# Kernel optimization log

Measured on AMD Instinct MI355X. Metric: run time of the kernel, lower is better.

The kernel has to match this reference:

```python
import jax, jax.numpy as jnp
import numpy as np

B_SZ, SEQ, ENC = 8, 768, 21
PRED = 192
N_HIPPO = 256
MULTISCALE = [1, 2, 4]
MODES = 32  # min(32, min(pred_len, seq_len)//2)


def _transition(N):
    Q = np.arange(N, dtype=np.float64)
    R = (2 * Q + 1)[:, None]
    j, i = np.meshgrid(Q, Q)
    A = np.where(i < j, -1.0, (-1.0) ** (i - j + 1)) * R
    Bv = (-1.0) ** Q[:, None] * R
    return A, Bv


def _hippo_discrete(N, dt):
    # scipy cont2discrete bilinear (Tustin, alpha=0.5)
    A, Bv = _transition(N)
    I = np.eye(N)
    M = I - (dt / 2.0) * A
    Ad = np.linalg.solve(M, I + (dt / 2.0) * A)
    Bd = np.linalg.solve(M, dt * Bv).squeeze(-1)
    return (jnp.asarray(Ad, jnp.float32), jnp.asarray(Bd, jnp.float32))


def _eval_matrix(N, dt):
    # ss.eval_legendre(arange(N)[:,None], 1-2*vals).T  -> (len(vals), N)
    vals = np.arange(0.0, 1.0, dt)
    x = 1.0 - 2.0 * vals
    P = np.zeros((len(vals), N), dtype=np.float64)
    P[:, 0] = 1.0
    if N > 1:
        P[:, 1] = x
    for n in range(1, N - 1):
        P[:, n + 1] = ((2 * n + 1) * x * P[:, n] - n * P[:, n - 1]) / (n + 1)
    return jnp.asarray(P, jnp.float32)


def _legt(x, A, Bv):
    # x: (B, E, L) -> HiPPO coeffs (B, E, N, L) via linear recurrence
    fs = jnp.moveaxis(x, -1, 0)  # (L, B, E)
    c0 = jnp.zeros(x.shape[:-1] + (A.shape[0],), x.dtype)

    def step(c, f):
        c = c @ A.T + f[..., None] * Bv
        return c, c

    _, cs = jax.lax.scan(step, c0, fs)  # (L, B, E, N)
    return jnp.moveaxis(cs, 0, -1)  # (B, E, N, L)


def _spectral(x, wr, wi):
    # x: (B, E, N_in, L); wr/wi: (N_in, N_out, MODES)
    L = x.shape[-1]
    xft = jnp.fft.rfft(x)
    a = xft[..., :MODES]
    o_re = jnp.einsum('bjix,iox->bjox', a.real, wr) - jnp.einsum('bjix,iox->bjox', a.imag, wi)
    o_im = jnp.einsum('bjix,iox->bjox', a.real, wi) + jnp.einsum('bjix,iox->bjox', a.imag, wr)
    o = jax.lax.complex(o_re, o_im)
    pad = jnp.zeros(o.shape[:-1] + (L // 2 + 1 - MODES,), o.dtype)
    return jnp.fft.irfft(jnp.concatenate([o, pad], axis=-1), n=L)


def _forward(x_enc, affine_weight, affine_bias, spec_wr, spec_wi, mlp_w, mlp_b):
    means = jax.lax.stop_gradient(jnp.mean(x_enc, axis=1, keepdims=True))
    xc = x_enc - means
    stdev = jax.lax.stop_gradient(jnp.sqrt(jnp.var(xc, axis=1, keepdims=True) + 1e-5))
    xc = xc / stdev
    xc = xc * affine_weight + affine_bias

    x_decs = []
    for i, m in enumerate(MULTISCALE):
        dt = 1.0 / PRED / m
        A, Bv = _hippo_discrete(N_HIPPO, dt)
        ev = _eval_matrix(N_HIPPO, dt)  # (m*PRED, N)
        x_in = xc[:, -m * PRED:]  # (B, L, E)
        c = _legt(jnp.transpose(x_in, (0, 2, 1)), A, Bv)  # (B, E, N, L)
        out1 = _spectral(c, spec_wr[i], spec_wi[i])  # (B, E, N, L)
        # seq_len >= pred_len branch: take time index PRED-1 along L
        x_dec_c = out1[:, :, :, PRED - 1].swapaxes(-1, -1)  # (B, E, N) after transpose(2,3) + index
        x_dec_c = out1.swapaxes(2, 3)[:, :, PRED - 1, :]  # (B, E, N)
        x_dec = x_dec_c @ ev[-PRED:, :].T  # (B, E, PRED)
        x_decs.append(x_dec)

    xd = jnp.stack(x_decs, axis=-1)  # (B, E, PRED, 3)
    xd = jnp.einsum('beps,os->bepo', xd, mlp_w) + mlp_b  # Linear(3,1)
    xd = jnp.transpose(xd[..., 0], (0, 2, 1))  # (B, PRED, E)
    xd = (xd - affine_bias) / (affine_weight + 1e-10)
    xd = xd * stdev + means
    return xd


def setup_inputs() -> dict:
    key = jax.random.key(0)
    ks = jax.random.split(key, 8)
    scale = 1.0 / (N_HIPPO * N_HIPPO)
    return {
        'x_enc': jax.random.normal(ks[0], (B_SZ, SEQ, ENC), jnp.float32),
        'x_mark_enc': jax.random.normal(ks[1], (B_SZ, SEQ, 4), jnp.float32),
        'x_dec_true': jax.random.normal(ks[2], (B_SZ, 240, ENC), jnp.float32),
        'x_mark_dec': jax.random.normal(ks[3], (B_SZ, 240, 4), jnp.float32),
        'affine_weight': jnp.ones((1, 1, ENC), jnp.float32),
        'affine_bias': jnp.zeros((1, 1, ENC), jnp.float32),
        'spec_wr': scale * jax.random.uniform(ks[4], (3, N_HIPPO, N_HIPPO, MODES), jnp.float32),
        'spec_wi': scale * jax.random.uniform(ks[5], (3, N_HIPPO, N_HIPPO, MODES), jnp.float32),
        'mlp_w': jax.random.normal(ks[6], (1, 3), jnp.float32) * 0.3,
        'mlp_b': jnp.zeros((1,), jnp.float32),
    }


def reference(x_enc, x_mark_enc, x_dec_true, x_mark_dec, affine_weight, affine_bias,
              spec_wr, spec_wi, mlp_w, mlp_b):
    # x_mark_enc / x_dec_true / x_mark_dec are unused by the forecast path (as in torch).
    return _forward(x_enc, affine_weight, affine_bias, spec_wr, spec_wi, mlp_w, mlp_b)
```

## Files before the change

### kernel.cpp

```cpp
#include <hip/hip_runtime.h>
#include <vector>
#include <cmath>
#include <cstring>

#define PI_D 3.14159265358979323846

typedef unsigned short ushort_t;
typedef __attribute__((ext_vector_type(8))) short bf16x8;
typedef __attribute__((ext_vector_type(4))) float f32x4;

#define CF_TRIG_F 0
#define CF_EVP_F  192
#define CF_FLOATS 147648
#define CU_USHORTS 688128
#define CONST_BYTES (CF_FLOATS*4 + CU_USHORTS*2)

#define OFF_XCT   0
#define OFF_MEANS 129024
#define OFF_STD   129280
#define OFF_OUT1  129536
#define OFF_XP1P  258560
#define OFF_PART  1161728
#define OFF_AHI   5290496
#define OFF_ALO   9419264
#define OFF_FB2   13548032
#define OFF_YF    26130944
#define OFF_CFALL 40581632

static const int L_S[3] = {192, 384, 768};


static inline unsigned short h_f2b(float v) {
  unsigned int u; memcpy(&u, &v, 4);
  unsigned int r = (u + 0x7FFF + ((u >> 16) & 1)) >> 16;
  return (unsigned short)r;
}
static inline float h_b2f(unsigned short h) {
  unsigned int u = (unsigned int)h << 16; float f; memcpy(&f, &u, 4); return f;
}

static unsigned char g_consts[CONST_BYTES];

static void compute_consts_host(unsigned char* blob) {
  float* outf = (float*)blob;
  ushort_t* outu = (ushort_t*)(blob + CF_FLOATS * 4);
  const int N = 256;
  for (int s = 0; s < 3; ++s) {
    const int L = L_S[s];
    const int m = 1 << s;
    const double dt = 1.0 / 192.0 / (double)m;

    for (int k = 0; k < 32; ++k) {
      double th = 2.0 * PI_D * (double)k * 191.0 / (double)L;
      outf[CF_TRIG_F + s * 64 + 2 * k]     = (float)cos(th);
      outf[CF_TRIG_F + s * 64 + 2 * k + 1] = (float)sin(th);
    }
    for (int r = 0; r < 192; ++r) {
      int irow = L - 192 + r;
      double x = 1.0 - 2.0 * ((double)irow * dt);
      float* dst = outf + CF_EVP_F + ((size_t)s * 192 + r) * 256;
      double pm1 = 1.0, pc = x;
      dst[0] = 1.0f; dst[1] = (float)x;
      for (int n = 1; n < N - 1; ++n) {
        double pn = ((2.0 * n + 1.0) * x * pc - (double)n * pm1) / (double)(n + 1);
        pm1 = pc; pc = pn;
        dst[n + 1] = (float)pn;
      }
    }
    const int W = N + 257;
    std::vector<double> G((size_t)N * W);
    for (int i = 0; i < N; ++i) {
      double R = 2.0 * i + 1.0;
      for (int j = 0; j < N; ++j) {
        double a = (i < j) ? -R : ((((i - j + 1) & 1) ? -R : R));
        G[(size_t)i * W + j]     = (i == j ? 1.0 : 0.0) - 0.5 * dt * a;
        G[(size_t)i * W + N + j] = (i == j ? 1.0 : 0.0) + 0.5 * dt * a;
      }
      G[(size_t)i * W + N + 256] = dt * (((i & 1) ? -R : R));
    }
    for (int k = 0; k < N; ++k) {
      int piv = k; double best = fabs(G[(size_t)k * W + k]);
      for (int r = k + 1; r < N; ++r) {
        double v = fabs(G[(size_t)r * W + k]);
        if (v > best) { best = v; piv = r; }
      }
      if (piv != k)
        for (int c = k; c < W; ++c) std::swap(G[(size_t)k * W + c], G[(size_t)piv * W + c]);
      double inv = 1.0 / G[(size_t)k * W + k];
      for (int r = k + 1; r < N; ++r) {
        double f = G[(size_t)r * W + k] * inv;
        if (f != 0.0) {
          double* Rr = &G[(size_t)r * W];
          const double* Rk = &G[(size_t)k * W];
          for (int c = k; c < W; ++c) Rr[c] -= f * Rk[c];
        }
      }
    }
    std::vector<double> X((size_t)N * 257);
    for (int k = N - 1; k >= 0; --k) {
      double inv = 1.0 / G[(size_t)k * W + k];
      const double* Rk = &G[(size_t)k * W];
      for (int c = 0; c < 257; ++c) {
        double v = Rk[N + c];
        for (int j = k + 1; j < N; ++j) v -= Rk[j] * X[(size_t)j * 257 + c];
        X[(size_t)k * 257 + c] = v * inv;
      }
    }
    std::vector<double> Ad((size_t)N * N), kvec(N), knew(N);
    for (int i = 0; i < N; ++i)
      for (int j = 0; j < N; ++j)
        Ad[(size_t)i * N + j] = (double)(float)X[(size_t)i * 257 + j];
    for (int i = 0; i < N; ++i) kvec[i] = (double)(float)X[(size_t)i * 257 + 256];

    ushort_t* fkt = outu + 98304 * ((1 << s) - 1);
    for (int d = 0; d < L; ++d) {
      if (d > 0) {
        for (int i = 0; i < N; ++i) {
          const double* row = &Ad[(size_t)i * N];
          double acc = 0.0;
          for (int j = 0; j < N; ++j) acc += row[j] * kvec[j];
          knew[i] = acc;
        }
        kvec.swap(knew);
      }
      for (int n = 0; n < N; ++n) {
        float kv = (float)kvec[n];
        unsigned short hi = h_f2b(kv);
        unsigned short lo = h_f2b(kv - h_b2f(hi));
        size_t base = ((size_t)((d >> 5) * 16 + (n >> 4)) * 2) * 512
                    + (size_t)((d & 31) >> 3) * 128 + (size_t)(n & 15) * 8 + (d & 7);
        fkt[base]       = hi;
        fkt[base + 512] = lo;
      }
    }
  }
}

static bool  g_dev_ok  = false;
static void* g_dev_ptr = nullptr;

namespace {
struct ConstInit {
  ConstInit() {
    compute_consts_host(g_consts);
    void* p = nullptr;
    if (hipMalloc(&p, CONST_BYTES) == hipSuccess && p != nullptr) {
      if (hipMemcpy(p, g_consts, CONST_BYTES, hipMemcpyHostToDevice) == hipSuccess) {
        g_dev_ptr = p;
        g_dev_ok  = true;
      } else {
        (void)hipFree(p);
      }
    }
    (void)hipHostRegister((void*)g_consts, sizeof(g_consts), hipHostRegisterDefault);
  }
};
static ConstInit g_const_init;
}

__device__ inline unsigned short f2b(float v) {
  unsigned int u = __float_as_uint(v);
  unsigned int r = (u + 0x7FFF + ((u >> 16) & 1)) >> 16;
  return (unsigned short)r;
}
__device__ inline float b2f(unsigned short h) {
  return __uint_as_float((unsigned int)h << 16);
}
__device__ inline unsigned int pack2(float a, float b) {
  return (unsigned int)f2b(a) | ((unsigned int)f2b(b) << 16);
}

__device__ inline float blockReduceSum(float v) {
  __shared__ float sm[4];
  #pragma unroll
  for (int off = 32; off > 0; off >>= 1) v += __shfl_down(v, off);
  int wid = threadIdx.x >> 6, lane = threadIdx.x & 63;
  if (lane == 0) sm[wid] = v;
  __syncthreads();
  if (threadIdx.x == 0) sm[0] = sm[0] + sm[1] + sm[2] + sm[3];
  __syncthreads();
  float r = sm[0];
  __syncthreads();
  return r;
}

__global__ __launch_bounds__(256) void norm_kernel(
    const float* __restrict__ x_enc, const float* __restrict__ aw,
    const float* __restrict__ ab, float* __restrict__ xcT,
    float* __restrict__ means, float* __restrict__ stdev) {
  int bj = blockIdx.x; int b = bj / 21, j = bj % 21;
  const float* xp = x_enc + (size_t)b * 768 * 21 + j;
  int tid = threadIdx.x;
  float lv[3]; float s = 0.f;
  #pragma unroll
  for (int i = 0; i < 3; ++i) { lv[i] = xp[(size_t)(tid + 256 * i) * 21]; s += lv[i]; }
  float tot = blockReduceSum(s);
  float mean = tot * (1.0f / 768.0f);
  float v = 0.f;
  #pragma unroll
  for (int i = 0; i < 3; ++i) { float d = lv[i] - mean; v += d * d; }
  float totv = blockReduceSum(v);
  float sd = sqrtf(totv * (1.0f / 768.0f) + 1e-5f);
  if (tid == 0) { means[bj] = mean; stdev[bj] = sd; }
  float wj = aw[j], bjv = ab[j];
  #pragma unroll
  for (int i = 0; i < 3; ++i)
    xcT[(size_t)bj * 768 + tid + 256 * i] = ((lv[i] - mean) / sd) * wj + bjv;
}

__global__ __launch_bounds__(256) void xp1_kernel(
    const float* __restrict__ xcT, double2* __restrict__ P) {
  int tid = blockIdx.x * 256 + threadIdx.x;
  if (tid >= 5376 * 42) return;
  int nk = tid % 5376, cg = tid / 5376;
  int scale = (cg < 6) ? 0 : (cg < 18 ? 1 : 2);
  int c = cg - 6 * ((1 << scale) - 1);
  int L = 192 << scale;
  int bj = nk >> 5, k = nk & 31;
  const float* x = xcT + (size_t)bj * 768 + (768 - L);
  int u0 = c * 32;
  double ang = -2.0 * PI_D * (double)((k * u0) % L) / (double)L;
  float re = (float)cos(ang), im = (float)sin(ang);
  double wang = -2.0 * PI_D * (double)k / (double)L;
  float cw = (float)cos(wang), sw = (float)sin(wang);
  double sre = 0.0, sim = 0.0;
  #pragma unroll 8
  for (int j = 0; j < 32; ++j) {
    float xv = x[u0 + j];
    sre += (double)(xv * re); sim += (double)(xv * im);
    float nr = re * cw - im * sw, ni = re * sw + im * cw;
    re = nr; im = ni;
  }
  P[(size_t)cg * 5376 + nk] = make_double2(sre, sim);
}

__global__ __launch_bounds__(256) void xp2_kernel(
    const float* __restrict__ xcT, const double2* __restrict__ P,
    ushort_t* __restrict__ YF) {
  int tid = blockIdx.x * 256 + threadIdx.x;
  if (tid >= 5376 * 42) return;
  int nk = tid % 5376, cg = tid / 5376;
  int scale = (cg < 6) ? 0 : (cg < 18 ? 1 : 2);
  int cbase = 6 * ((1 << scale) - 1);
  int c = cg - cbase;
  int L = 192 << scale;
  ushort_t* FA = YF + (size_t)4128768 * ((1 << scale) - 1);
  int bj = nk >> 5, k = nk & 31;
  const float* x = xcT + (size_t)bj * 768 + (768 - L);
  double bre = 0.0, bim = 0.0;
  for (int cc = cbase; cc < cg; ++cc) {
    double2 p = P[(size_t)cc * 5376 + nk];
    bre += p.x; bim += p.y;
  }
  int u0 = c * 32;
  double ang = -2.0 * PI_D * (double)((k * u0) % L) / (double)L;
  float ure = (float)cos(ang), uim = (float)sin(ang);
  double wang = -2.0 * PI_D * (double)k / (double)L;
  float cw = (float)cos(wang), sw = (float)sin(wang);
  int d0 = L - 1 - u0;
  double angd = -2.0 * PI_D * (double)((k * d0) % L) / (double)L;
  float dre = (float)cos(angd), dim = (float)sin(angd);

  float vre_buf[32], vim_buf[32];
  #pragma unroll
  for (int j = 0; j < 32; ++j) {
    float xv = x[u0 + j];
    bre += (double)(xv * ure); bim += (double)(xv * uim);
    float brf = (float)bre, bif = (float)bim;
    int m = 31 - j;
    vre_buf[m] = dre * brf - dim * bif;
    vim_buf[m] = dre * bif + dim * brf;
    float t1 = ure * cw - uim * sw, t2 = ure * sw + uim * cw;
    ure = t1; uim = t2;
    float t3 = dre * cw + dim * sw, t4 = dim * cw - dre * sw;
    dre = t3; dim = t4;
  }

  int nK0 = L >> 5;
  int K0 = (d0 - 31) >> 5;
  int rre = bj * 64 + k * 2;
  int rim = rre + 1;
  size_t baseRe = (((size_t)(rre >> 4) * nK0 + K0) * 2) * 512 + (size_t)(rre & 15) * 8;
  size_t baseIm = (((size_t)(rim >> 4) * nK0 + K0) * 2) * 512 + (size_t)(rim & 15) * 8;
  #pragma unroll
  for (int q = 0; q < 4; ++q) {
    float f0 = vre_buf[q*8+0], f1 = vre_buf[q*8+1], f2 = vre_buf[q*8+2], f3 = vre_buf[q*8+3];
    float f4 = vre_buf[q*8+4], f5 = vre_buf[q*8+5], f6 = vre_buf[q*8+6], f7 = vre_buf[q*8+7];
    uint4 vh = make_uint4(pack2(f0,f1), pack2(f2,f3), pack2(f4,f5), pack2(f6,f7));
    uint4 vl = make_uint4(pack2(f0-b2f(f2b(f0)), f1-b2f(f2b(f1))),
                          pack2(f2-b2f(f2b(f2)), f3-b2f(f2b(f3))),
                          pack2(f4-b2f(f2b(f4)), f5-b2f(f2b(f5))),
                          pack2(f6-b2f(f2b(f6)), f7-b2f(f2b(f7))));
    *(uint4*)(FA + baseRe + q*128)       = vh;
    *(uint4*)(FA + baseRe + 512 + q*128) = vl;
  }
  #pragma unroll
  for (int q = 0; q < 4; ++q) {
    float f0 = vim_buf[q*8+0], f1 = vim_buf[q*8+1], f2 = vim_buf[q*8+2], f3 = vim_buf[q*8+3];
    float f4 = vim_buf[q*8+4], f5 = vim_buf[q*8+5], f6 = vim_buf[q*8+6], f7 = vim_buf[q*8+7];
    uint4 vh = make_uint4(pack2(f0,f1), pack2(f2,f3), pack2(f4,f5), pack2(f6,f7));
    uint4 vl = make_uint4(pack2(f0-b2f(f2b(f0)), f1-b2f(f2b(f1))),
                          pack2(f2-b2f(f2b(f2)), f3-b2f(f2b(f3))),
                          pack2(f4-b2f(f2b(f4)), f5-b2f(f2b(f5))),
                          pack2(f6-b2f(f2b(f6)), f7-b2f(f2b(f7))));
    *(uint4*)(FA + baseIm + q*128)       = vh;
    *(uint4*)(FA + baseIm + 512 + q*128) = vl;
  }
}

__global__ __launch_bounds__(768, 3) void gemm1_wb(
    const ushort_t* __restrict__ YF, const ushort_t* __restrict__ KTall,
    ushort_t* __restrict__ AHI, ushort_t* __restrict__ ALO,
    const float* __restrict__ wrS_all, const float* __restrict__ wiS_all,
    const float* __restrict__ trig_all, ushort_t* __restrict__ FB2_all) {
  if (blockIdx.x < 384) {
    if (threadIdx.x >= 512) return;
    int wbid = blockIdx.x;
    int of  = wbid & 15;
    int nsb = (wbid >> 4) & 7;
    int s   = wbid >> 7;
    const float* wrS = wrS_all + (size_t)s * 256 * 256 * 32;
    const float* wiS = wiS_all + (size_t)s * 256 * 256 * 32;
    const float* trig = trig_all + s * 64;
    ushort_t* FB2 = FB2_all + (size_t)s * 8388608;
    int L = 192 << s;
    int t = threadIdx.x;
    int lgk = t >> 7;
    int e   = t & 7;
    int om  = (t >> 3) & 15;
    int nstate = nsb * 32 + lgk * 8 + e;
    int o = of * 16 + om;
    const float* wrp = wrS + ((size_t)nstate * 256 + o) * 32;
    const float* wip = wiS + ((size_t)nstate * 256 + o) * 32;
    float invL = 1.0f / (float)L;
    #pragma unroll 4
    for (int k = 0; k < 32; ++k) {
      float ck = trig[2 * k], sk = trig[2 * k + 1];
      float fk = (k == 0 ? 1.0f : 2.0f) * invL;
      float wr = wrp[k], wi = wip[k];
      float vre = fk * (wr * ck - wi * sk);
      float vim = fk * (-wi * ck - wr * sk);
      int qre = (k * 2) * 8 + nsb;
      size_t bre = ((size_t)(qre * 16 + of) * 2) * 512 + t;
      size_t bim = ((size_t)((qre + 8) * 16 + of) * 2) * 512 + t;
      unsigned short hre = f2b(vre), him = f2b(vim);
      FB2[bre]       = hre;
      FB2[bre + 512] = f2b(vre - b2f(hre));
      FB2[bim]       = him;
      FB2[bim + 512] = f2b(vim - b2f(him));
    }
    return;
  }

  const int gb = blockIdx.x - 384;
  const int s = gb / 112;
  const int bx = gb % 112;
  const int K = 192 << s;
  const ushort_t* FA = YF + (size_t)4128768 * ((1 << s) - 1);
  const ushort_t* FB = KTall + (size_t)98304 * ((1 << s) - 1);
  ushort_t* Chi = AHI + (size_t)2752512 * s;
  ushort_t* Clo = ALO + (size_t)2752512 * s;

  const int wave = threadIdx.x >> 6;
  const int lane = threadIdx.x & 63;
  const int li = lane & 15, lg = lane >> 4;
  const int mh = wave >> 2;
  const int nw = wave & 3;
  const int bn = nw * 64;
  const int nK0 = K >> 5;
  const int strip = bx * 6 + mh * 2;
  const int nf0 = nw * 4;

  bf16x8 aH0[2], aL0[2], bH0[4], bL0[4];
  bf16x8 aH1[2], aL1[2], bH1[4], bL1[4];
  f32x4 acc[2][4] = {};

  #define G1_LOAD(AH, AL, BH, BL, K0_) {                                      \
    _Pragma("unroll")                                                         \
    for (int st = 0; st < 2; ++st) {                                          \
      size_t fa = ((size_t)((strip + st) * nK0 + (K0_)) * 2) * 512 + lane * 8;\
      AH[st] = *(const bf16x8*)(FA + fa);                                     \
      AL[st] = *(const bf16x8*)(FA + fa + 512);                               \
    }                                                                         \
    _Pragma("unroll")                                                         \
    for (int nf = 0; nf < 4; ++nf) {                                          \
      size_t fb = ((size_t)((K0_) * 16 + nf0 + nf) * 2) * 512 + lane * 8;     \
      BH[nf] = *(const bf16x8*)(FB + fb);                                     \
      BL[nf] = *(const bf16x8*)(FB + fb + 512);                               \
    } }

  #define G1_MFMA(AH, AL, BH, BL) {                                          \
    _Pragma("unroll")                                                        \
    for (int st = 0; st < 2; ++st)                                           \
      _Pragma("unroll")                                                      \
      for (int nf = 0; nf < 4; ++nf) {                                       \
        acc[st][nf] = __builtin_amdgcn_mfma_f32_16x16x32_bf16(AH[st], BH[nf], acc[st][nf], 0, 0, 0); \
        acc[st][nf] = __builtin_amdgcn_mfma_f32_16x16x32_bf16(AH[st], BL[nf], acc[st][nf], 0, 0, 0); \
        acc[st][nf] = __builtin_amdgcn_mfma_f32_16x16x32_bf16(AL[st], BH[nf], acc[st][nf], 0, 0, 0); \
      } }

  G1_LOAD(aH0, aL0, bH0, bL0, 0);
  for (int K0 = 0; K0 < nK0; K0 += 2) {
    G1_LOAD(aH1, aL1, bH1, bL1, K0 + 1);
    G1_MFMA(aH0, aL0, bH0, bL0);
    if (K0 + 2 < nK0) G1_LOAD(aH0, aL0, bH0, bL0, K0 + 2);
    G1_MFMA(aH1, aL1, bH1, bL1);
  }
  #undef G1_LOAD
  #undef G1_MFMA

  #pragma unroll
  for (int st = 0; st < 2; ++st) {
    #pragma unroll
    for (int r = 0; r < 4; ++r) {
      int row = (strip + st) * 16 + lg * 4 + r;
      #pragma unroll
      for (int nf = 0; nf < 4; ++nf) {
        int col = bn + nf * 16 + li;
        float v = acc[st][nf][r];
        unsigned short hi = f2b(v);
        Chi[(size_t)row * 256 + col] = hi;
        Clo[(size_t)row * 256 + col] = f2b(v - b2f(hi));
      }
    }
  }
}

__global__ __launch_bounds__(256) void gemm2_mfma(
    const ushort_t* __restrict__ AHI, const ushort_t* __restrict__ ALO,
    const ushort_t* __restrict__ FB2_all, float* __restrict__ PART) {
  const int zz = blockIdx.z;
  const int s = zz >> 5;
  const int z = zz & 31;
  const ushort_t* Ahi = AHI + (size_t)2752512 * s;
  const ushort_t* Alo = ALO + (size_t)2752512 * s;
  const ushort_t* FB2 = FB2_all + (size_t)s * 8388608;
  float* C = PART + (size_t)s * 1376256 + (size_t)z * 43008;

  const int wave = threadIdx.x >> 6;
  const int lane = threadIdx.x & 63;
  const int li = lane & 15, lg = lane >> 4;
  const int bm = blockIdx.y * 64;
  const int bn = blockIdx.x * 64;
  const int nf0 = blockIdx.x * 4;
  const int ks = z * 512;

  const int rowA = bm + wave * 16 + li;
  const bool aok = (rowA < 168);
  const size_t aoff = (size_t)(aok ? rowA : 0) * 16384;

  bf16x8 aH0, aL0, bH0[4], bL0[4];
  bf16x8 aH1, aL1, bH1[4], bL1[4];
  f32x4 acc[4] = {};

  #define G2_LOAD(AH, AL, BH, BL, KC_) {                                   \
    int kc_ = (KC_) + lg * 8;                                              \
    if (aok) { AH = *(const bf16x8*)(Ahi + aoff + kc_);                    \
               AL = *(const bf16x8*)(Alo + aoff + kc_); }                  \
    else     { AH = (bf16x8)(short)0; AL = (bf16x8)(short)0; }             \
    int q_ = (KC_) >> 5;                                                   \
    _Pragma("unroll")                                                      \
    for (int nf = 0; nf < 4; ++nf) {                                       \
      size_t fb = ((size_t)(q_ * 16 + nf0 + nf) * 2) * 512 + lane * 8;     \
      BH[nf] = *(const bf16x8*)(FB2 + fb);                                 \
      BL[nf] = *(const bf16x8*)(FB2 + fb + 512);                           \
    } }

  #define G2_MFMA(AH, AL, BH, BL) {                                        \
    _Pragma("unroll")                                                      \
    for (int nf = 0; nf < 4; ++nf) {                                       \
      acc[nf] = __builtin_amdgcn_mfma_f32_16x16x32_bf16(AH, BH[nf], acc[nf], 0, 0, 0); \
      acc[nf] = __builtin_amdgcn_mfma_f32_16x16x32_bf16(AH, BL[nf], acc[nf], 0, 0, 0); \
      acc[nf] = __builtin_amdgcn_mfma_f32_16x16x32_bf16(AL, BH[nf], acc[nf], 0, 0, 0); \
    } }

  G2_LOAD(aH0, aL0, bH0, bL0, ks);
  for (int k0 = ks; k0 < ks + 512; k0 += 64) {
    G2_LOAD(aH1, aL1, bH1, bL1, k0 + 32);
    G2_MFMA(aH0, aL0, bH0, bL0);
    if (k0 + 64 < ks + 512) G2_LOAD(aH0, aL0, bH0, bL0, k0 + 64);
    G2_MFMA(aH1, aL1, bH1, bL1);
  }
  #undef G2_LOAD
  #undef G2_MFMA

  #pragma unroll
  for (int r = 0; r < 4; ++r) {
    int row = bm + wave * 16 + lg * 4 + r;
    if (row < 168) {
      #pragma unroll
      for (int nf = 0; nf < 4; ++nf) {
        int col = bn + nf * 16 + li;
        C[(size_t)row * 256 + col] = acc[nf][r];
      }
    }
  }
}

__global__ __launch_bounds__(256) void reduce_kernel(
    const float* __restrict__ PART, float* __restrict__ OUT1) {
  int s = blockIdx.y;
  int e = blockIdx.x * 256 + threadIdx.x;
  const float* part = PART + (size_t)s * 1376256;
  float sum = 0.f;
  for (int c = 0; c < 32; ++c) sum += part[(size_t)c * 43008 + e];
  OUT1[(size_t)s * 43008 + e] = sum;
}

__global__ __launch_bounds__(256) void final_kernel(
    const float* __restrict__ out1, const float* __restrict__ evp,
    const float* __restrict__ means, const float* __restrict__ stdev,
    const float* __restrict__ aw, const float* __restrict__ ab,
    const float* __restrict__ mlp_w, const float* __restrict__ mlp_b,
    float* __restrict__ out) {
  int tid = blockIdx.x * 256 + threadIdx.x;
  int j = tid % 21; int bp = tid / 21; int p = bp % 192; int b = bp / 192;
  int bj = b * 21 + j;
  float acc = mlp_b[0];
  #pragma unroll
  for (int s = 0; s < 3; ++s) {
    const float* o1 = out1 + ((size_t)s * 168 + bj) * 256;
    const float* ev = evp + ((size_t)s * 192 + p) * 256;
    float d = 0.f;
    #pragma unroll 4
    for (int n = 0; n < 256; ++n) d = fmaf(o1[n], ev[n], d);
    acc = fmaf(mlp_w[s], d, acc);
  }
  float v = (acc - ab[j]) / (aw[j] + 1e-10f);
  out[tid] = v * stdev[bj] + means[bj];
}

extern "C" void kernel_launch(void* const* d_in, const int* in_sizes, int n_in,
                              void* d_out, int out_size, void* d_ws, size_t ws_size,
                              hipStream_t stream) {
  const float* x_enc   = (const float*)d_in[0];
  const float* aw      = (const float*)d_in[4];
  const float* ab      = (const float*)d_in[5];
  const float* spec_wr = (const float*)d_in[6];
  const float* spec_wi = (const float*)d_in[7];
  const float* mlp_w   = (const float*)d_in[8];
  const float* mlp_b   = (const float*)d_in[9];
  float* wsf = (float*)d_ws;
  float* out = (float*)d_out;

  const unsigned char* cst_base;
  if (g_dev_ok) {
    cst_base = (const unsigned char*)g_dev_ptr;
  } else {
    hipMemcpyAsync(wsf + OFF_CFALL, g_consts, CONST_BYTES,
                   hipMemcpyHostToDevice, stream);
    cst_base = (const unsigned char*)(wsf + OFF_CFALL);
  }
  const float*    cst_f  = (const float*)cst_base;
  const ushort_t* cst_us = (const ushort_t*)(cst_base + CF_FLOATS * 4);

  ushort_t* yf  = (ushort_t*)(wsf + OFF_YF);
  ushort_t* ahi = (ushort_t*)(wsf + OFF_AHI);
  ushort_t* alo = (ushort_t*)(wsf + OFF_ALO);
  ushort_t* fb2 = (ushort_t*)(wsf + OFF_FB2);

  norm_kernel<<<168, 256, 0, stream>>>(x_enc, aw, ab,
      wsf + OFF_XCT, wsf + OFF_MEANS, wsf + OFF_STD);

  xp1_kernel<<<(5376 * 42 + 255) / 256, 256, 0, stream>>>(
      wsf + OFF_XCT, (double2*)(wsf + OFF_XP1P));
  xp2_kernel<<<(5376 * 42 + 255) / 256, 256, 0, stream>>>(
      wsf + OFF_XCT, (const double2*)(wsf + OFF_XP1P), yf);
  gemm1_wb<<<384 + 336, 768, 0, stream>>>(
      yf, cst_us, ahi, alo,
      spec_wr, spec_wi, cst_f + CF_TRIG_F, fb2);
  gemm2_mfma<<<dim3(4, 3, 96), 256, 0, stream>>>(
      ahi, alo, fb2, wsf + OFF_PART);
  reduce_kernel<<<dim3(168, 3), 256, 0, stream>>>(
      wsf + OFF_PART, wsf + OFF_OUT1);

  final_kernel<<<126, 256, 0, stream>>>(
      wsf + OFF_OUT1, cst_f + CF_EVP_F, wsf + OFF_MEANS, wsf + OFF_STD,
      aw, ab, mlp_w, mlp_b, out);
}
```

Baseline: 179.4 us.

## Stage shared B operand tiles in LDS with double-buffered async loads

The GEMM branch of gemm1_wb now has all 12 waves cooperatively copy each K-step's B tile (hi and lo bf16 fragments) from global memory into a double-buffered shared-memory array using global_load_lds. Waves then read B from LDS rather than each loading it separately from global memory. The goal is to remove redundant global loads of B across the waves that share it. In exchange it adds a block-wide barrier every K step, drops the register double-buffering of A, and uses 64 KB of LDS with launch bounds lowered from 3 to 2 blocks per CU, which reduces occupancy for both branches of the kernel.

```diff
diff --git a/kernel.cpp b/kernel.cpp
--- a/kernel.cpp
+++ b/kernel.cpp
@@ -28,7 +28,6 @@
 #define OFF_CFALL 40581632
 
 static const int L_S[3] = {192, 384, 768};
-
 
 static inline unsigned short h_f2b(float v) {
   unsigned int u; memcpy(&u, &v, 4);
@@ -308,11 +307,13 @@
   }
 }
 
-__global__ __launch_bounds__(768, 3) void gemm1_wb(
+__global__ __launch_bounds__(768, 2) void gemm1_wb(
     const ushort_t* __restrict__ YF, const ushort_t* __restrict__ KTall,
     ushort_t* __restrict__ AHI, ushort_t* __restrict__ ALO,
     const float* __restrict__ wrS_all, const float* __restrict__ wiS_all,
     const float* __restrict__ trig_all, ushort_t* __restrict__ FB2_all) {
+  __shared__ ushort_t Bs[2][16384];
+
   if (blockIdx.x < 384) {
     if (threadIdx.x >= 512) return;
     int wbid = blockIdx.x;
@@ -371,43 +372,46 @@
   const int strip = bx * 6 + mh * 2;
   const int nf0 = nw * 4;
 
-  bf16x8 aH0[2], aL0[2], bH0[4], bL0[4];
-  bf16x8 aH1[2], aL1[2], bH1[4], bL1[4];
+  #define STAGE_B(CUR, K0_) {                                                 \
+    for (int f = wave; f < 32; f += 12) {                                     \
+      const ushort_t* gsrc = FB                                               \
+          + ((size_t)((K0_) * 16 + (f >> 1)) * 2 + (f & 1)) * 512 + lane * 8; \
+      __builtin_amdgcn_global_load_lds(                                       \
+          (const __attribute__((address_space(1))) void*)gsrc,                \
+          (__attribute__((address_space(3))) void*)&Bs[CUR][f * 512],         \
+          16, 0, 0);                                                          \
+    } }
+
+  bf16x8 aH[2], aL[2];
   f32x4 acc[2][4] = {};
 
-  #define G1_LOAD(AH, AL, BH, BL, K0_) {                                      \
-    _Pragma("unroll")                                                         \
-    for (int st = 0; st < 2; ++st) {                                          \
-      size_t fa = ((size_t)((strip + st) * nK0 + (K0_)) * 2) * 512 + lane * 8;\
-      AH[st] = *(const bf16x8*)(FA + fa);                                     \
-      AL[st] = *(const bf16x8*)(FA + fa + 512);                               \
-    }                                                                         \
-    _Pragma("unroll")                                                         \
-    for (int nf = 0; nf < 4; ++nf) {                                          \
-      size_t fb = ((size_t)((K0_) * 16 + nf0 + nf) * 2) * 512 + lane * 8;     \
-      BH[nf] = *(const bf16x8*)(FB + fb);                                     \
-      BL[nf] = *(const bf16x8*)(FB + fb + 512);                               \
-    } }
-
-  #define G1_MFMA(AH, AL, BH, BL) {                                          \
-    _Pragma("unroll")                                                        \
-    for (int st = 0; st < 2; ++st)                                           \
-      _Pragma("unroll")                                                      \
-      for (int nf = 0; nf < 4; ++nf) {                                       \
-        acc[st][nf] = __builtin_amdgcn_mfma_f32_16x16x32_bf16(AH[st], BH[nf], acc[st][nf], 0, 0, 0); \
-        acc[st][nf] = __builtin_amdgcn_mfma_f32_16x16x32_bf16(AH[st], BL[nf], acc[st][nf], 0, 0, 0); \
-        acc[st][nf] = __builtin_amdgcn_mfma_f32_16x16x32_bf16(AL[st], BH[nf], acc[st][nf], 0, 0, 0); \
-      } }
-
-  G1_LOAD(aH0, aL0, bH0, bL0, 0);
-  for (int K0 = 0; K0 < nK0; K0 += 2) {
-    G1_LOAD(aH1, aL1, bH1, bL1, K0 + 1);
-    G1_MFMA(aH0, aL0, bH0, bL0);
-    if (K0 + 2 < nK0) G1_LOAD(aH0, aL0, bH0, bL0, K0 + 2);
-    G1_MFMA(aH1, aL1, bH1, bL1);
-  }
-  #undef G1_LOAD
-  #undef G1_MFMA
+  STAGE_B(0, 0);
+  __syncthreads();
+
+  int cur = 0;
+  for (int K0 = 0; K0 < nK0; ++K0) {
+    #pragma unroll
+    for (int st = 0; st < 2; ++st) {
+      size_t fa = ((size_t)((strip + st) * nK0 + K0) * 2) * 512 + lane * 8;
+      aH[st] = *(const bf16x8*)(FA + fa);
+      aL[st] = *(const bf16x8*)(FA + fa + 512);
+    }
+    if (K0 + 1 < nK0) STAGE_B(cur ^ 1, K0 + 1);
+    #pragma unroll
+    for (int nf = 0; nf < 4; ++nf) {
+      bf16x8 bh = *(const bf16x8*)&Bs[cur][((nf0 + nf) * 2 + 0) * 512 + lane * 8];
+      bf16x8 bl = *(const bf16x8*)&Bs[cur][((nf0 + nf) * 2 + 1) * 512 + lane * 8];
+      #pragma unroll
+      for (int st = 0; st < 2; ++st) {
+        acc[st][nf] = __builtin_amdgcn_mfma_f32_16x16x32_bf16(aH[st], bh, acc[st][nf], 0, 0, 0);
+        acc[st][nf] = __builtin_amdgcn_mfma_f32_16x16x32_bf16(aH[st], bl, acc[st][nf], 0, 0, 0);
+        acc[st][nf] = __builtin_amdgcn_mfma_f32_16x16x32_bf16(aL[st], bh, acc[st][nf], 0, 0, 0);
+      }
+    }
+    __syncthreads();
+    cur ^= 1;
+  }
+  #undef STAGE_B
 
   #pragma unroll
   for (int st = 0; st < 2; ++st) {
```

Result: no change. 179.6 us (+0.1%).
